# Performance work log

Measured on AMD Instinct MI355X. Metric: run time of the kernel, lower is better.

Reference implementation:

```python
import jax, jax.numpy as jnp
import numpy as np

B, T = 32, 2000
ENC2, DEC, ATTN = 1024, 512, 512
NUM_KERNEL, KW, PAD = 10, 100, 50


def setup_inputs() -> dict:
    key = jax.random.key(0)
    ks = jax.random.split(key, 10)
    enc_output = jax.random.normal(ks[0], (B, T, ENC2), dtype=jnp.float32)
    prev_dec_hidden = jax.random.normal(ks[1], (B, DEC), dtype=jnp.float32)
    a = jax.random.uniform(ks[2], (B, 1, T), dtype=jnp.float32)
    prev_alpha = a / jnp.sum(a, axis=2, keepdims=True)
    mask = jnp.ones((B, T), dtype=jnp.float32)
    # parameters (torch Linear weight [out,in] stored transposed as [in,out])
    W_conv = jax.random.normal(ks[3], (NUM_KERNEL, 1, KW), dtype=jnp.float32) * 0.1
    W_c2s = jax.random.normal(ks[4], (NUM_KERNEL, ATTN), dtype=jnp.float32) * 0.1
    W_enc = jax.random.normal(ks[5], (ENC2, ATTN), dtype=jnp.float32) * 0.03
    b_enc = jax.random.normal(ks[6], (ATTN,), dtype=jnp.float32) * 0.03
    W_dec = jax.random.normal(ks[7], (DEC, ATTN), dtype=jnp.float32) * 0.04
    w_score = jax.random.normal(ks[8], (ATTN,), dtype=jnp.float32) * 0.04
    return {"enc_output": enc_output, "prev_dec_hidden": prev_dec_hidden,
            "prev_alpha": prev_alpha, "mask": mask,
            "W_conv": W_conv, "W_c2s": W_c2s, "W_enc": W_enc, "b_enc": b_enc,
            "W_dec": W_dec, "w_score": w_score}


def reference(enc_output, prev_dec_hidden, prev_alpha, mask,
              W_conv, W_c2s, W_enc, b_enc, W_dec, w_score):
    Tlen = enc_output.shape[1]
    # location conv: [B,1,T] -> [B,num_kernel,T+1] (even kernel + symmetric pad)
    conv = jax.lax.conv_general_dilated(
        prev_alpha, W_conv, window_strides=(1,), padding=[(PAD, PAD)],
        dimension_numbers=("NCH", "OIH", "NCH"))
    tmpconv = jnp.transpose(conv, (0, 2, 1))[:, :Tlen, :]        # [B,T,K]
    prev_attn_e = jnp.einsum("btk,ka->bta", tmpconv, W_c2s)      # [B,T,A]
    enc_e = jnp.einsum("bte,ea->bta", enc_output, W_enc) + b_enc  # [B,T,A]
    dec_e = (prev_dec_hidden @ W_dec)[:, None, :]                 # [B,1,A]
    e = jnp.tanh(enc_e + dec_e + prev_attn_e)                     # [B,T,A]
    e = jnp.einsum("bta,a->bt", e, w_score)                       # [B,T]
    e_exp = jnp.exp(e - jnp.max(e, axis=1, keepdims=True)) * mask
    alpha = e_exp / jnp.sum(e_exp, axis=1, keepdims=True)
    return alpha[:, None, :]                                      # [B,1,T]
```

## Files before the change

kernel.cpp:

```cpp
#include <hip/hip_runtime.h>
#include <math.h>

#define Bn    32
#define Tn    2000
#define Mrows (Bn * Tn)
#define ENC2n 1024
#define ATTNn 512
#define DECn  512
#define NKn   10
#define KWn   100
#define PADn  50

#define OFF_DB    (Mrows * NKn)
#define OFF_SCORE (OFF_DB + Bn * ATTNn)
#define OFF_WT    (OFF_SCORE + Mrows)

typedef _Float16 v8h __attribute__((ext_vector_type(8)));
typedef float f32x4 __attribute__((ext_vector_type(4)));

__device__ __forceinline__ float fast_tanh(float v) {
  const float e = __expf(2.f * v);
  return 1.f - 2.f * __builtin_amdgcn_rcpf(e + 1.f);
}

__global__ __launch_bounds__(256) void k_wt(const float* __restrict__ W,
                                            _Float16* __restrict__ Wt) {
  __shared__ float sh[32][33];
  const int x = threadIdx.x & 31, y = threadIdx.x >> 5;
  const int k0 = blockIdx.x * 32, c0 = blockIdx.y * 32;
  for (int i = y; i < 32; i += 8) sh[i][x] = W[(size_t)(k0 + i) * ATTNn + c0 + x];
  __syncthreads();
  for (int i = y; i < 32; i += 8)
    Wt[(size_t)(c0 + i) * ENC2n + k0 + x] = (_Float16)sh[x][i];
}

__global__ __launch_bounds__(256) void k_conv(const float* __restrict__ alpha,
                                              const float* __restrict__ Wconv,
                                              float* __restrict__ ws) {
  __shared__ float sh[256 + KWn - 1];
  __shared__ float wc[NKn * KWn];
  const int b = blockIdx.y;
  const int t0 = blockIdx.x * 256;
  const int tid = threadIdx.x;

  for (int i = tid; i < NKn * KWn; i += 256) wc[i] = Wconv[i];
  const float* __restrict__ arow = alpha + b * Tn;
  for (int i = tid; i < 256 + KWn - 1; i += 256) {
    const int t = t0 - PADn + i;
    sh[i] = (t >= 0 && t < Tn) ? arow[t] : 0.f;
  }
  __syncthreads();

  const int t = t0 + tid;
  if (t < Tn) {
    float acc[NKn];
#pragma unroll
    for (int k = 0; k < NKn; ++k) acc[k] = 0.f;
    for (int i = 0; i < KWn; ++i) {
      const float a = sh[tid + i];
#pragma unroll
      for (int k = 0; k < NKn; ++k) acc[k] = fmaf(a, wc[k * KWn + i], acc[k]);
    }
    float* tp = ws + (size_t)(b * Tn + t) * NKn;
#pragma unroll
    for (int k = 0; k < NKn; ++k) tp[k] = acc[k];
    ws[OFF_SCORE + b * Tn + t] = 0.f;
  }
}

__global__ __launch_bounds__(512) void k_dec(const float* __restrict__ h,
                                             const float* __restrict__ Wdec,
                                             const float* __restrict__ benc,
                                             float* __restrict__ ws) {
  __shared__ float sh[DECn];
  const int b = blockIdx.x;
  const int a = threadIdx.x;
  sh[a] = h[b * DECn + a];
  __syncthreads();
  float acc = 0.f;
  for (int d = 0; d < DECn; ++d) acc = fmaf(sh[d], Wdec[d * ATTNn + a], acc);
  ws[OFF_DB + b * ATTNn + a] = benc[a] + acc;
}

#define BM 128
#define BN 128
#define BK 32
#define LDKh 40
#define NT (ENC2n / BK)

#define LOADT(Pa0, Pa1, Pa2, Pa3, Pw0, Pw1, kn)     \
  Pa0 = *(const float4*)(asrc + (kn));              \
  Pa1 = *(const float4*)(asrc + (kn) + 4);          \
  Pa2 = *(const float4*)(asrc + (kn) + 8);          \
  Pa3 = *(const float4*)(asrc + (kn) + 12);         \
  Pw0 = *(const v8h*)(wsrc + (kn));                 \
  Pw1 = *(const v8h*)(wsrc + (kn) + 8);

#define STORET(buf, Pa0, Pa1, Pa2, Pa3, Pw0, Pw1) {                          \
  v8h h0, h1;                                                                \
  h0[0]=(_Float16)Pa0.x; h0[1]=(_Float16)Pa0.y; h0[2]=(_Float16)Pa0.z;       \
  h0[3]=(_Float16)Pa0.w; h0[4]=(_Float16)Pa1.x; h0[5]=(_Float16)Pa1.y;       \
  h0[6]=(_Float16)Pa1.z; h0[7]=(_Float16)Pa1.w;                              \
  h1[0]=(_Float16)Pa2.x; h1[1]=(_Float16)Pa2.y; h1[2]=(_Float16)Pa2.z;       \
  h1[3]=(_Float16)Pa2.w; h1[4]=(_Float16)Pa3.x; h1[5]=(_Float16)Pa3.y;       \
  h1[6]=(_Float16)Pa3.z; h1[7]=(_Float16)Pa3.w;                              \
  *(v8h*)&Asl[buf][sr][sk]     = h0;                                         \
  *(v8h*)&Asl[buf][sr][sk + 8] = h1;                                         \
  *(v8h*)&Wsl[buf][sr][sk]     = Pw0;                                        \
  *(v8h*)&Wsl[buf][sr][sk + 8] = Pw1; }

#define COMPUTET(buf) {                                                      \
  v8h af[4], bf[4];                                                          \
  _Pragma("unroll")                                                          \
  for (int m = 0; m < 4; ++m)                                                \
    af[m] = *(const v8h*)&Asl[buf][wm * 64 + m * 16 + lr][kk];               \
  _Pragma("unroll")                                                          \
  for (int n = 0; n < 4; ++n)                                                \
    bf[n] = *(const v8h*)&Wsl[buf][wn * 64 + n * 16 + lr][kk];               \
  __builtin_amdgcn_s_setprio(1);                                             \
  _Pragma("unroll")                                                          \
  for (int m = 0; m < 4; ++m)                                                \
    _Pragma("unroll")                                                        \
    for (int n = 0; n < 4; ++n)                                              \
      acc[m][n] = __builtin_amdgcn_mfma_f32_16x16x32_f16(af[m], bf[n],       \
                                                         acc[m][n], 0, 0, 0);\
  __builtin_amdgcn_s_setprio(0); }

#define BARRIER() {                                                          \
  asm volatile("s_waitcnt lgkmcnt(0)" ::: "memory");                         \
  __builtin_amdgcn_s_barrier(); }

__global__ __launch_bounds__(256, 3) void k_main(
    const float* __restrict__ A,
    const _Float16* __restrict__ Wt,
    const float* __restrict__ Wc2s,
    const float* __restrict__ wscore,
    float* __restrict__ ws) {
  __shared__ _Float16 Asl[2][BM][LDKh];
  __shared__ _Float16 Wsl[2][BN][LDKh];
  const int tid = threadIdx.x;
  const int lane = tid & 63;
  const int wv = tid >> 6;
  const int wm = wv >> 1, wn = wv & 1;

  const int l = blockIdx.x;
  const int lp = (l & 7) * 250 + (l >> 3);
  const int row0 = (lp >> 2) * BM;
  const int c0 = (lp & 3) * BN;

  const int sr = tid >> 1, sk = (tid & 1) * 16;
  const float* __restrict__ asrc = A + (size_t)(row0 + sr) * ENC2n + sk;
  const _Float16* __restrict__ wsrc = Wt + (size_t)(c0 + sr) * ENC2n + sk;

  const int lr = lane & 15, lg = lane >> 4;
  const int kk = lg * 8;

  f32x4 acc[4][4];
#pragma unroll
  for (int m = 0; m < 4; ++m)
#pragma unroll
    for (int n = 0; n < 4; ++n) acc[m][n] = (f32x4)0.f;

  float4 xa0, xa1, xa2, xa3; v8h xw0, xw1;
  float4 ya0, ya1, ya2, ya3; v8h yw0, yw1;

  LOADT(xa0, xa1, xa2, xa3, xw0, xw1, 0);
  LOADT(ya0, ya1, ya2, ya3, yw0, yw1, BK);
  STORET(0, xa0, xa1, xa2, xa3, xw0, xw1);
  BARRIER();

  for (int t = 0; t < NT - 2; t += 2) {
    LOADT(xa0, xa1, xa2, xa3, xw0, xw1, (t + 2) * BK);
    COMPUTET(0);
    STORET(1, ya0, ya1, ya2, ya3, yw0, yw1);
    BARRIER();
    LOADT(ya0, ya1, ya2, ya3, yw0, yw1, (t + 3) * BK);
    COMPUTET(1);
    STORET(0, xa0, xa1, xa2, xa3, xw0, xw1);
    BARRIER();
  }
  COMPUTET(0);
  STORET(1, ya0, ya1, ya2, ya3, yw0, yw1);
  BARRIER();
  COMPUTET(1);

  __syncthreads();
  float* tcs = (float*)&Asl[0][0][0];
  {
    const float* __restrict__ tsrc = ws + (size_t)row0 * NKn;
    for (int i = tid; i < BM * NKn; i += 256) tcs[i] = tsrc[i];
  }
  __syncthreads();

  const float* __restrict__ DB = ws + OFF_DB;
  float wc2[4][NKn], wsc[4];
  int cl[4];
#pragma unroll
  for (int fn = 0; fn < 4; ++fn) {
    cl[fn] = c0 + wn * 64 + fn * 16 + lr;
    wsc[fn] = wscore[cl[fn]];
#pragma unroll
    for (int k = 0; k < NKn; ++k) wc2[fn][k] = Wc2s[k * ATTNn + cl[fn]];
  }

#pragma unroll
  for (int fm = 0; fm < 4; ++fm) {
#pragma unroll
    for (int r = 0; r < 4; ++r) {
      const int rowL = wm * 64 + fm * 16 + lg * 4 + r;
      const int grow = row0 + rowL;
      const int b = grow / Tn;
      const float* __restrict__ tk = &tcs[rowL * NKn];
      float tkv[NKn];
#pragma unroll
      for (int k = 0; k < NKn; ++k) tkv[k] = tk[k];
      float p = 0.f;
#pragma unroll
      for (int fn = 0; fn < 4; ++fn) {
        float v = acc[fm][fn][r] + DB[b * ATTNn + cl[fn]];
#pragma unroll
        for (int k = 0; k < NKn; ++k) v = fmaf(tkv[k], wc2[fn][k], v);
        p = fmaf(wsc[fn], fast_tanh(v), p);
      }
      p += __shfl_down(p, 8, 16);
      p += __shfl_down(p, 4, 16);
      p += __shfl_down(p, 2, 16);
      p += __shfl_down(p, 1, 16);
      if (lr == 0) atomicAdd(&ws[OFF_SCORE + grow], p);
    }
  }
}

__global__ __launch_bounds__(256) void k_softmax(const float* __restrict__ ws,
                                                 const float* __restrict__ mask,
                                                 float* __restrict__ out) {
  const int b = blockIdx.x, tid = threadIdx.x;
  const float* __restrict__ s = ws + OFF_SCORE + b * Tn;
  const float* __restrict__ mrow = mask + b * Tn;
  float* __restrict__ orow = out + b * Tn;
  __shared__ float red[4];

  float m = -1e30f;
  for (int t = tid; t < Tn; t += 256) m = fmaxf(m, s[t]);
#pragma unroll
  for (int off = 32; off; off >>= 1) m = fmaxf(m, __shfl_down(m, off));
  if ((tid & 63) == 0) red[tid >> 6] = m;
  __syncthreads();
  m = fmaxf(fmaxf(red[0], red[1]), fmaxf(red[2], red[3]));
  __syncthreads();

  float sum = 0.f;
  for (int t = tid; t < Tn; t += 256) {
    const float e = expf(s[t] - m) * mrow[t];
    orow[t] = e;
    sum += e;
  }
#pragma unroll
  for (int off = 32; off; off >>= 1) sum += __shfl_down(sum, off);
  if ((tid & 63) == 0) red[tid >> 6] = sum;
  __syncthreads();
  sum = red[0] + red[1] + red[2] + red[3];
  const float inv = 1.f / sum;
  for (int t = tid; t < Tn; t += 256) orow[t] *= inv;
}

extern "C" void kernel_launch(void* const* d_in, const int* in_sizes, int n_in,
                              void* d_out, int out_size, void* d_ws, size_t ws_size,
                              hipStream_t stream) {
  const float* enc   = (const float*)d_in[0];
  const float* hid   = (const float*)d_in[1];
  const float* alpha = (const float*)d_in[2];
  const float* mask  = (const float*)d_in[3];
  const float* Wconv = (const float*)d_in[4];
  const float* Wc2s  = (const float*)d_in[5];
  const float* Wenc  = (const float*)d_in[6];
  const float* benc  = (const float*)d_in[7];
  const float* Wdec  = (const float*)d_in[8];
  const float* wscr  = (const float*)d_in[9];
  float* out = (float*)d_out;
  float* ws  = (float*)d_ws;
  _Float16* Wt = (_Float16*)(ws + OFF_WT);

  k_wt<<<dim3(ENC2n / 32, ATTNn / 32), 256, 0, stream>>>(Wenc, Wt);
  k_conv<<<dim3((Tn + 255) / 256, Bn), 256, 0, stream>>>(alpha, Wconv, ws);
  k_dec<<<Bn, DECn, 0, stream>>>(hid, Wdec, benc, ws);
  k_main<<<2000, 256, 0, stream>>>(enc, Wt, Wc2s, wscr, ws);
  k_softmax<<<Bn, 256, 0, stream>>>(ws, mask, out);
}
```

Measured before the change: 199.2 us.

## Pre-convert encoder to fp16 and stream GEMM tiles via direct global-to-LDS loads

Adds a pass that converts the full fp32 encoder output to fp16 in workspace. The GEMM then loads A and W tiles directly into LDS with global_load_lds in MFMA-fragment order, using a triple-buffered pipeline. Blocks shrink to 2 waves, each computing 128x64 with more accumulators. This removes register staging and in-loop conversion, but adds a full extra read of the 262MB fp32 input and a 131MB fp16 write, which is large for a memory-bound problem. Each output tile also re-reads the A rows four times.

```diff
diff --git a/kernel.cpp b/kernel.cpp
--- a/kernel.cpp
+++ b/kernel.cpp
@@ -14,6 +14,7 @@
 #define OFF_DB    (Mrows * NKn)
 #define OFF_SCORE (OFF_DB + Bn * ATTNn)
 #define OFF_WT    (OFF_SCORE + Mrows)
+#define OFF_AF16  (OFF_WT + 262144)
 
 typedef _Float16 v8h __attribute__((ext_vector_type(8)));
 typedef float f32x4 __attribute__((ext_vector_type(4)));
@@ -21,6 +22,12 @@
 __device__ __forceinline__ float fast_tanh(float v) {
   const float e = __expf(2.f * v);
   return 1.f - 2.f * __builtin_amdgcn_rcpf(e + 1.f);
+}
+
+__device__ __forceinline__ void gload_lds16(const void* g, void* l) {
+  __builtin_amdgcn_global_load_lds(
+      (const __attribute__((address_space(1))) void*)g,
+      (__attribute__((address_space(3))) void*)l, 16, 0, 0);
 }
 
 __global__ __launch_bounds__(256) void k_wt(const float* __restrict__ W,
@@ -32,6 +39,23 @@
   __syncthreads();
   for (int i = y; i < 32; i += 8)
     Wt[(size_t)(c0 + i) * ENC2n + k0 + x] = (_Float16)sh[x][i];
+}
+
+__global__ __launch_bounds__(256) void k_acvt(const float* __restrict__ A,
+                                              _Float16* __restrict__ Af) {
+  const size_t total = (size_t)Mrows * ENC2n;
+  const size_t stride = (size_t)gridDim.x * 256 * 8;
+  for (size_t i = ((size_t)blockIdx.x * 256 + threadIdx.x) * 8; i < total;
+       i += stride) {
+    const float4 a = *(const float4*)(A + i);
+    const float4 b = *(const float4*)(A + i + 4);
+    v8h h;
+    h[0] = (_Float16)a.x; h[1] = (_Float16)a.y;
+    h[2] = (_Float16)a.z; h[3] = (_Float16)a.w;
+    h[4] = (_Float16)b.x; h[5] = (_Float16)b.y;
+    h[6] = (_Float16)b.z; h[7] = (_Float16)b.w;
+    *(v8h*)(Af + i) = h;
+  }
 }
 
 __global__ __launch_bounds__(256) void k_conv(const float* __restrict__ alpha,
@@ -85,129 +109,112 @@
 #define BM 128
 #define BN 128
 #define BK 32
-#define LDKh 40
 #define NT (ENC2n / BK)
 
-#define LOADT(Pa0, Pa1, Pa2, Pa3, Pw0, Pw1, kn)     \
-  Pa0 = *(const float4*)(asrc + (kn));              \
-  Pa1 = *(const float4*)(asrc + (kn) + 4);          \
-  Pa2 = *(const float4*)(asrc + (kn) + 8);          \
-  Pa3 = *(const float4*)(asrc + (kn) + 12);         \
-  Pw0 = *(const v8h*)(wsrc + (kn));                 \
-  Pw1 = *(const v8h*)(wsrc + (kn) + 8);
-
-#define STORET(buf, Pa0, Pa1, Pa2, Pa3, Pw0, Pw1) {                          \
-  v8h h0, h1;                                                                \
-  h0[0]=(_Float16)Pa0.x; h0[1]=(_Float16)Pa0.y; h0[2]=(_Float16)Pa0.z;       \
-  h0[3]=(_Float16)Pa0.w; h0[4]=(_Float16)Pa1.x; h0[5]=(_Float16)Pa1.y;       \
-  h0[6]=(_Float16)Pa1.z; h0[7]=(_Float16)Pa1.w;                              \
-  h1[0]=(_Float16)Pa2.x; h1[1]=(_Float16)Pa2.y; h1[2]=(_Float16)Pa2.z;       \
-  h1[3]=(_Float16)Pa2.w; h1[4]=(_Float16)Pa3.x; h1[5]=(_Float16)Pa3.y;       \
-  h1[6]=(_Float16)Pa3.z; h1[7]=(_Float16)Pa3.w;                              \
-  *(v8h*)&Asl[buf][sr][sk]     = h0;                                         \
-  *(v8h*)&Asl[buf][sr][sk + 8] = h1;                                         \
-  *(v8h*)&Wsl[buf][sr][sk]     = Pw0;                                        \
-  *(v8h*)&Wsl[buf][sr][sk + 8] = Pw1; }
-
-#define COMPUTET(buf) {                                                      \
-  v8h af[4], bf[4];                                                          \
+#define DMAW(wb, kt) {                                                       \
+  gload_lds16(aW0 + (kt) * BK, &Wb[wb][(4 * wv + 0) * 512]);                 \
+  gload_lds16(aW1 + (kt) * BK, &Wb[wb][(4 * wv + 1) * 512]);                 \
+  gload_lds16(aW2 + (kt) * BK, &Wb[wb][(4 * wv + 2) * 512]);                 \
+  gload_lds16(aW3 + (kt) * BK, &Wb[wb][(4 * wv + 3) * 512]); }
+
+#define DMAA(ab, kt) {                                                       \
+  gload_lds16(aA0 + (kt) * BK, &Ab[ab][(4 * wv + 0) * 512]);                 \
+  gload_lds16(aA1 + (kt) * BK, &Ab[ab][(4 * wv + 1) * 512]);                 \
+  gload_lds16(aA2 + (kt) * BK, &Ab[ab][(4 * wv + 2) * 512]);                 \
+  gload_lds16(aA3 + (kt) * BK, &Ab[ab][(4 * wv + 3) * 512]); }
+
+#define COMPUTE(buf) {                                                       \
+  v8h af[8], bf[4];                                                          \
   _Pragma("unroll")                                                          \
-  for (int m = 0; m < 4; ++m)                                                \
-    af[m] = *(const v8h*)&Asl[buf][wm * 64 + m * 16 + lr][kk];               \
+  for (int m = 0; m < 8; ++m)                                                \
+    af[m] = *(const v8h*)&Ab[buf][m * 512 + lane * 8];                       \
   _Pragma("unroll")                                                          \
   for (int n = 0; n < 4; ++n)                                                \
-    bf[n] = *(const v8h*)&Wsl[buf][wn * 64 + n * 16 + lr][kk];               \
+    bf[n] = *(const v8h*)&Wb[buf][(4 * wv + n) * 512 + lane * 8];            \
   __builtin_amdgcn_s_setprio(1);                                             \
   _Pragma("unroll")                                                          \
-  for (int m = 0; m < 4; ++m)                                                \
+  for (int m = 0; m < 8; ++m)                                                \
     _Pragma("unroll")                                                        \
     for (int n = 0; n < 4; ++n)                                              \
       acc[m][n] = __builtin_amdgcn_mfma_f32_16x16x32_f16(af[m], bf[n],       \
                                                          acc[m][n], 0, 0, 0);\
   __builtin_amdgcn_s_setprio(0); }
 
-#define BARRIER() {                                                          \
-  asm volatile("s_waitcnt lgkmcnt(0)" ::: "memory");                         \
+#define BARN(N) {                                                            \
+  asm volatile("s_waitcnt vmcnt(" #N ") lgkmcnt(0)" ::: "memory");           \
   __builtin_amdgcn_s_barrier(); }
 
-__global__ __launch_bounds__(256, 3) void k_main(
-    const float* __restrict__ A,
+__global__ __launch_bounds__(128, 2) void k_main(
+    const _Float16* __restrict__ Af,
     const _Float16* __restrict__ Wt,
     const float* __restrict__ Wc2s,
     const float* __restrict__ wscore,
     float* __restrict__ ws) {
-  __shared__ _Float16 Asl[2][BM][LDKh];
-  __shared__ _Float16 Wsl[2][BN][LDKh];
+  __shared__ _Float16 Ab[3][4096];
+  __shared__ _Float16 Wb[3][4096];
   const int tid = threadIdx.x;
   const int lane = tid & 63;
   const int wv = tid >> 6;
-  const int wm = wv >> 1, wn = wv & 1;
 
   const int l = blockIdx.x;
   const int lp = (l & 7) * 250 + (l >> 3);
   const int row0 = (lp >> 2) * BM;
   const int c0 = (lp & 3) * BN;
 
-  const int sr = tid >> 1, sk = (tid & 1) * 16;
-  const float* __restrict__ asrc = A + (size_t)(row0 + sr) * ENC2n + sk;
-  const _Float16* __restrict__ wsrc = Wt + (size_t)(c0 + sr) * ENC2n + sk;
-
-  const int lr = lane & 15, lg = lane >> 4;
-  const int kk = lg * 8;
-
-  f32x4 acc[4][4];
-#pragma unroll
-  for (int m = 0; m < 4; ++m)
+  const int lsub = (lane & 15), ksl = (lane >> 4) * 8;
+  const _Float16* aA0 = Af + (size_t)(row0 + (4 * wv + 0) * 16 + lsub) * ENC2n + ksl;
+  const _Float16* aA1 = Af + (size_t)(row0 + (4 * wv + 1) * 16 + lsub) * ENC2n + ksl;
+  const _Float16* aA2 = Af + (size_t)(row0 + (4 * wv + 2) * 16 + lsub) * ENC2n + ksl;
+  const _Float16* aA3 = Af + (size_t)(row0 + (4 * wv + 3) * 16 + lsub) * ENC2n + ksl;
+  const _Float16* aW0 = Wt + (size_t)(c0 + (4 * wv + 0) * 16 + lsub) * ENC2n + ksl;
+  const _Float16* aW1 = Wt + (size_t)(c0 + (4 * wv + 1) * 16 + lsub) * ENC2n + ksl;
+  const _Float16* aW2 = Wt + (size_t)(c0 + (4 * wv + 2) * 16 + lsub) * ENC2n + ksl;
+  const _Float16* aW3 = Wt + (size_t)(c0 + (4 * wv + 3) * 16 + lsub) * ENC2n + ksl;
+
+  f32x4 acc[8][4];
+#pragma unroll
+  for (int m = 0; m < 8; ++m)
 #pragma unroll
     for (int n = 0; n < 4; ++n) acc[m][n] = (f32x4)0.f;
 
-  float4 xa0, xa1, xa2, xa3; v8h xw0, xw1;
-  float4 ya0, ya1, ya2, ya3; v8h yw0, yw1;
-
-  LOADT(xa0, xa1, xa2, xa3, xw0, xw1, 0);
-  LOADT(ya0, ya1, ya2, ya3, yw0, yw1, BK);
-  STORET(0, xa0, xa1, xa2, xa3, xw0, xw1);
-  BARRIER();
-
-  for (int t = 0; t < NT - 2; t += 2) {
-    LOADT(xa0, xa1, xa2, xa3, xw0, xw1, (t + 2) * BK);
-    COMPUTET(0);
-    STORET(1, ya0, ya1, ya2, ya3, yw0, yw1);
-    BARRIER();
-    LOADT(ya0, ya1, ya2, ya3, yw0, yw1, (t + 3) * BK);
-    COMPUTET(1);
-    STORET(0, xa0, xa1, xa2, xa3, xw0, xw1);
-    BARRIER();
-  }
-  COMPUTET(0);
-  STORET(1, ya0, ya1, ya2, ya3, yw0, yw1);
-  BARRIER();
-  COMPUTET(1);
-
-  __syncthreads();
-  float* tcs = (float*)&Asl[0][0][0];
+  DMAW(0, 0); DMAA(0, 0);
+  DMAW(1, 1); DMAA(1, 1);
+  BARN(8);
+
+  for (int t3 = 0; t3 < 30; t3 += 3) {
+    DMAW(2, t3 + 2); DMAA(2, t3 + 2); COMPUTE(0); BARN(8);
+    DMAW(0, t3 + 3); DMAA(0, t3 + 3); COMPUTE(1); BARN(8);
+    DMAW(1, t3 + 4); DMAA(1, t3 + 4); COMPUTE(2); BARN(8);
+  }
+  COMPUTE(0);
+  BARN(0);
+  COMPUTE(1);
+
+  __syncthreads();
+  float* tcs = (float*)&Ab[0][0];
   {
     const float* __restrict__ tsrc = ws + (size_t)row0 * NKn;
-    for (int i = tid; i < BM * NKn; i += 256) tcs[i] = tsrc[i];
+    for (int i = tid; i < BM * NKn; i += 128) tcs[i] = tsrc[i];
   }
   __syncthreads();
 
   const float* __restrict__ DB = ws + OFF_DB;
+  const int lr = lane & 15, lg = lane >> 4;
   float wc2[4][NKn], wsc[4];
   int cl[4];
 #pragma unroll
   for (int fn = 0; fn < 4; ++fn) {
-    cl[fn] = c0 + wn * 64 + fn * 16 + lr;
+    cl[fn] = c0 + wv * 64 + fn * 16 + lr;
     wsc[fn] = wscore[cl[fn]];
 #pragma unroll
     for (int k = 0; k < NKn; ++k) wc2[fn][k] = Wc2s[k * ATTNn + cl[fn]];
   }
 
 #pragma unroll
-  for (int fm = 0; fm < 4; ++fm) {
+  for (int fm = 0; fm < 8; ++fm) {
 #pragma unroll
     for (int r = 0; r < 4; ++r) {
-      const int rowL = wm * 64 + fm * 16 + lg * 4 + r;
+      const int rowL = fm * 16 + lg * 4 + r;
       const int grow = row0 + rowL;
       const int b = grow / Tn;
       const float* __restrict__ tk = &tcs[rowL * NKn];
@@ -280,10 +287,12 @@
   float* out = (float*)d_out;
   float* ws  = (float*)d_ws;
   _Float16* Wt = (_Float16*)(ws + OFF_WT);
+  _Float16* Af = (_Float16*)(ws + OFF_AF16);
 
   k_wt<<<dim3(ENC2n / 32, ATTNn / 32), 256, 0, stream>>>(Wenc, Wt);
   k_conv<<<dim3((Tn + 255) / 256, Bn), 256, 0, stream>>>(alpha, Wconv, ws);
   k_dec<<<Bn, DECn, 0, stream>>>(hid, Wdec, benc, ws);
-  k_main<<<2000, 256, 0, stream>>>(enc, Wt, Wc2s, wscr, ws);
+  k_acvt<<<4096, 256, 0, stream>>>(enc, Af);
+  k_main<<<2000, 128, 0, stream>>>(Af, Wt, Wc2s, wscr, ws);
   k_softmax<<<Bn, 256, 0, stream>>>(ws, mask, out);
 }
```

Result: slower. 327.0 us (+64.2%).

## Stream fp16 weight tiles straight to LDS with triple buffering and XOR swizzle

Applied to the files above, without the earlier changes.

The GEMM main loop now copies the pre-transposed fp16 weight tiles from global memory directly into LDS with global_load_lds, which removes the register staging and ds_write for that operand. The weight buffer becomes triple-buffered and both LDS tiles switch from padded rows to an XOR-swizzled unpadded layout to avoid bank conflicts. The activation operand is still loaded through registers and converted to fp16. The loop is unrolled in six-phase groups with explicit vmcnt waits so loads overlap MFMA work. The cost is more complex index math, a larger LDS footprint, and a dependence on exact vmcnt counting for correctness.

```diff
diff --git a/kernel.cpp b/kernel.cpp
--- a/kernel.cpp
+++ b/kernel.cpp
@@ -23,6 +23,12 @@
   return 1.f - 2.f * __builtin_amdgcn_rcpf(e + 1.f);
 }
 
+__device__ __forceinline__ void gload_lds16(const void* g, void* l) {
+  __builtin_amdgcn_global_load_lds(
+      (const __attribute__((address_space(1))) void*)g,
+      (__attribute__((address_space(3))) void*)l, 16, 0, 0);
+}
+
 __global__ __launch_bounds__(256) void k_wt(const float* __restrict__ W,
                                             _Float16* __restrict__ Wt) {
   __shared__ float sh[32][33];
@@ -85,38 +91,39 @@
 #define BM 128
 #define BN 128
 #define BK 32
-#define LDKh 40
 #define NT (ENC2n / BK)
 
-#define LOADT(Pa0, Pa1, Pa2, Pa3, Pw0, Pw1, kn)     \
-  Pa0 = *(const float4*)(asrc + (kn));              \
-  Pa1 = *(const float4*)(asrc + (kn) + 4);          \
-  Pa2 = *(const float4*)(asrc + (kn) + 8);          \
-  Pa3 = *(const float4*)(asrc + (kn) + 12);         \
-  Pw0 = *(const v8h*)(wsrc + (kn));                 \
-  Pw1 = *(const v8h*)(wsrc + (kn) + 8);
-
-#define STORET(buf, Pa0, Pa1, Pa2, Pa3, Pw0, Pw1) {                          \
+#define LOADA(P, kt)                                  \
+  (P##0) = *(const float4*)(asrc + (kt) * BK);        \
+  (P##1) = *(const float4*)(asrc + (kt) * BK + 4);    \
+  (P##2) = *(const float4*)(asrc + (kt) * BK + 8);    \
+  (P##3) = *(const float4*)(asrc + (kt) * BK + 12);
+
+#define CVTSTORE(P, ab) {                                                    \
   v8h h0, h1;                                                                \
-  h0[0]=(_Float16)Pa0.x; h0[1]=(_Float16)Pa0.y; h0[2]=(_Float16)Pa0.z;       \
-  h0[3]=(_Float16)Pa0.w; h0[4]=(_Float16)Pa1.x; h0[5]=(_Float16)Pa1.y;       \
-  h0[6]=(_Float16)Pa1.z; h0[7]=(_Float16)Pa1.w;                              \
-  h1[0]=(_Float16)Pa2.x; h1[1]=(_Float16)Pa2.y; h1[2]=(_Float16)Pa2.z;       \
-  h1[3]=(_Float16)Pa2.w; h1[4]=(_Float16)Pa3.x; h1[5]=(_Float16)Pa3.y;       \
-  h1[6]=(_Float16)Pa3.z; h1[7]=(_Float16)Pa3.w;                              \
-  *(v8h*)&Asl[buf][sr][sk]     = h0;                                         \
-  *(v8h*)&Asl[buf][sr][sk + 8] = h1;                                         \
-  *(v8h*)&Wsl[buf][sr][sk]     = Pw0;                                        \
-  *(v8h*)&Wsl[buf][sr][sk + 8] = Pw1; }
-
-#define COMPUTET(buf) {                                                      \
+  h0[0] = (_Float16)(P##0).x; h0[1] = (_Float16)(P##0).y;                    \
+  h0[2] = (_Float16)(P##0).z; h0[3] = (_Float16)(P##0).w;                    \
+  h0[4] = (_Float16)(P##1).x; h0[5] = (_Float16)(P##1).y;                    \
+  h0[6] = (_Float16)(P##1).z; h0[7] = (_Float16)(P##1).w;                    \
+  h1[0] = (_Float16)(P##2).x; h1[1] = (_Float16)(P##2).y;                    \
+  h1[2] = (_Float16)(P##2).z; h1[3] = (_Float16)(P##2).w;                    \
+  h1[4] = (_Float16)(P##3).x; h1[5] = (_Float16)(P##3).y;                    \
+  h1[6] = (_Float16)(P##3).z; h1[7] = (_Float16)(P##3).w;                    \
+  *(v8h*)&Ab[ab][sw0] = h0;                                                  \
+  *(v8h*)&Ab[ab][sw1] = h1; }
+
+#define DMAW(wb, kt) {                                                       \
+  gload_lds16(wp0 + (kt) * BK, &Wb[wb][(wv * 2) * 512]);                     \
+  gload_lds16(wp1 + (kt) * BK, &Wb[wb][(wv * 2 + 1) * 512]); }
+
+#define COMPUTE(ab, wb) {                                                    \
   v8h af[4], bf[4];                                                          \
   _Pragma("unroll")                                                          \
   for (int m = 0; m < 4; ++m)                                                \
-    af[m] = *(const v8h*)&Asl[buf][wm * 64 + m * 16 + lr][kk];               \
+    af[m] = *(const v8h*)&Ab[ab][wm * 2048 + m * 512 + aoff];                \
   _Pragma("unroll")                                                          \
   for (int n = 0; n < 4; ++n)                                                \
-    bf[n] = *(const v8h*)&Wsl[buf][wn * 64 + n * 16 + lr][kk];               \
+    bf[n] = *(const v8h*)&Wb[wb][wn * 2048 + n * 512 + aoff];                \
   __builtin_amdgcn_s_setprio(1);                                             \
   _Pragma("unroll")                                                          \
   for (int m = 0; m < 4; ++m)                                                \
@@ -126,9 +133,20 @@
                                                          acc[m][n], 0, 0, 0);\
   __builtin_amdgcn_s_setprio(0); }
 
-#define BARRIER() {                                                          \
-  asm volatile("s_waitcnt lgkmcnt(0)" ::: "memory");                         \
+#define VMC(N) asm volatile("s_waitcnt vmcnt(" #N ")" ::: "memory");
+
+#define BARN(N) {                                                            \
+  asm volatile("s_waitcnt vmcnt(" #N ") lgkmcnt(0)" ::: "memory");           \
   __builtin_amdgcn_s_barrier(); }
+
+#define PHASE(ab, wc, wd, Pl, Pc, kt) {                                      \
+  LOADA(Pl, kt);                                                             \
+  DMAW(wd, kt);                                                              \
+  __builtin_amdgcn_sched_barrier(0);                                         \
+  COMPUTE(ab, wc);                                                           \
+  VMC(6);                                                                    \
+  CVTSTORE(Pc, (ab) ^ 1);                                                    \
+  BARN(6); }
 
 __global__ __launch_bounds__(256, 3) void k_main(
     const float* __restrict__ A,
@@ -136,8 +154,8 @@
     const float* __restrict__ Wc2s,
     const float* __restrict__ wscore,
     float* __restrict__ ws) {
-  __shared__ _Float16 Asl[2][BM][LDKh];
-  __shared__ _Float16 Wsl[2][BN][LDKh];
+  __shared__ _Float16 Ab[2][4096];
+  __shared__ _Float16 Wb[3][4096];
   const int tid = threadIdx.x;
   const int lane = tid & 63;
   const int wv = tid >> 6;
@@ -148,12 +166,29 @@
   const int row0 = (lp >> 2) * BM;
   const int c0 = (lp & 3) * BN;
 
-  const int sr = tid >> 1, sk = (tid & 1) * 16;
-  const float* __restrict__ asrc = A + (size_t)(row0 + sr) * ENC2n + sk;
-  const _Float16* __restrict__ wsrc = Wt + (size_t)(c0 + sr) * ENC2n + sk;
-
-  const int lr = lane & 15, lg = lane >> 4;
-  const int kk = lg * 8;
+  const int sr = tid >> 1, hh = tid & 1, mm = sr & 7;
+  const int u0 = sr * 4 + hh * 2;
+  const int sw0 = (u0 ^ mm) * 8;
+  const int sw1 = ((u0 + 1) ^ mm) * 8;
+  const float* __restrict__ asrc =
+      A + (size_t)(row0 + sr) * ENC2n + hh * 16;
+
+  const int aoff = ((((lane & 15) << 2) | (lane >> 4)) ^ (lane & 7)) * 8;
+
+  const _Float16* wp0;
+  const _Float16* wp1;
+  {
+    const int s0i = (wv * 2) * 64 + lane;
+    const int s1i = s0i + 64;
+    int s = s0i;
+    int rw = ((s >> 3) << 1) | (((s >> 2) ^ (s >> 4)) & 1);
+    int gg = ((((s >> 1) ^ (s >> 3)) & 1) << 1) | ((s ^ (s >> 2) ^ (s >> 4)) & 1);
+    wp0 = Wt + (size_t)(c0 + rw) * ENC2n + gg * 8;
+    s = s1i;
+    rw = ((s >> 3) << 1) | (((s >> 2) ^ (s >> 4)) & 1);
+    gg = ((((s >> 1) ^ (s >> 3)) & 1) << 1) | ((s ^ (s >> 2) ^ (s >> 4)) & 1);
+    wp1 = Wt + (size_t)(c0 + rw) * ENC2n + gg * 8;
+  }
 
   f32x4 acc[4][4];
 #pragma unroll
@@ -161,31 +196,33 @@
 #pragma unroll
     for (int n = 0; n < 4; ++n) acc[m][n] = (f32x4)0.f;
 
-  float4 xa0, xa1, xa2, xa3; v8h xw0, xw1;
-  float4 ya0, ya1, ya2, ya3; v8h yw0, yw1;
-
-  LOADT(xa0, xa1, xa2, xa3, xw0, xw1, 0);
-  LOADT(ya0, ya1, ya2, ya3, yw0, yw1, BK);
-  STORET(0, xa0, xa1, xa2, xa3, xw0, xw1);
-  BARRIER();
-
-  for (int t = 0; t < NT - 2; t += 2) {
-    LOADT(xa0, xa1, xa2, xa3, xw0, xw1, (t + 2) * BK);
-    COMPUTET(0);
-    STORET(1, ya0, ya1, ya2, ya3, yw0, yw1);
-    BARRIER();
-    LOADT(ya0, ya1, ya2, ya3, yw0, yw1, (t + 3) * BK);
-    COMPUTET(1);
-    STORET(0, xa0, xa1, xa2, xa3, xw0, xw1);
-    BARRIER();
-  }
-  COMPUTET(0);
-  STORET(1, ya0, ya1, ya2, ya3, yw0, yw1);
-  BARRIER();
-  COMPUTET(1);
-
-  __syncthreads();
-  float* tcs = (float*)&Asl[0][0][0];
+  float4 X0, X1, X2, X3, Y0, Y1, Y2, Y3;
+
+  LOADA(X, 0);
+  DMAW(0, 0);
+  LOADA(Y, 1);
+  DMAW(1, 1);
+  VMC(8);
+  CVTSTORE(X, 0);
+  BARN(6);
+
+  for (int it = 0; it < 5; ++it) {
+    const int k2 = it * 6 + 2;
+    PHASE(0, 0, 2, X, Y, k2 + 0);
+    PHASE(1, 1, 0, Y, X, k2 + 1);
+    PHASE(0, 2, 1, X, Y, k2 + 2);
+    PHASE(1, 0, 2, Y, X, k2 + 3);
+    PHASE(0, 1, 0, X, Y, k2 + 4);
+    PHASE(1, 2, 1, Y, X, k2 + 5);
+  }
+  COMPUTE(0, 0);
+  VMC(0);
+  CVTSTORE(Y, 1);
+  BARN(0);
+  COMPUTE(1, 1);
+
+  __syncthreads();
+  float* tcs = (float*)&Ab[0][0];
   {
     const float* __restrict__ tsrc = ws + (size_t)row0 * NKn;
     for (int i = tid; i < BM * NKn; i += 256) tcs[i] = tsrc[i];
@@ -193,6 +230,7 @@
   __syncthreads();
 
   const float* __restrict__ DB = ws + OFF_DB;
+  const int lr = lane & 15, lg = lane >> 4;
   float wc2[4][NKn], wsc[4];
   int cl[4];
 #pragma unroll
```

After: 261.0 us. 1.31x slower.
